# Performance work log

Measured on AMD Instinct MI355X. Metric: run time of the kernel, lower is better.

Reference implementation:

```python
import jax, jax.numpy as jnp
import numpy as np

L, F, LOG_T, NMIN, NMAX = 16, 2, 19, 16, 2048
T = 2 ** LOG_T
N_ROWS = 524288
PRIMES = np.array([1, 2654435761, 805459861], dtype=np.uint32)
# 8 corner offsets of the unit cube, bits (dx, dy, dz)
CORNERS = np.stack(np.meshgrid([0, 1], [0, 1], [0, 1], indexing='ij'), axis=-1).reshape(8, 3)


def setup_inputs() -> dict:
    key = jax.random.key(0)
    k1, k2 = jax.random.split(key)
    x = jax.random.uniform(k1, (N_ROWS, 3), dtype=jnp.float32)  # coords in [0,1)
    hashmap = jax.random.normal(k2, (L, F, T), dtype=jnp.float32) * 1e-2
    growth = np.exp((np.log(NMAX) - np.log(NMIN)) / (L - 1))
    resolution = jnp.asarray(np.floor(NMIN * growth ** np.arange(L)), dtype=jnp.float32)
    return {"x": x, "hashmap": hashmap, "resolution": resolution}


def _hash_encode(x, hashmap, resolution):
    # x: [n, 3], hashmap: [L, F, T], resolution: [L]
    n = x.shape[0]
    xs = x[:, None, :] * resolution[None, :, None]          # [n, L, 3]
    x0f = jnp.floor(xs)
    frac = xs - x0f                                          # trilinear fracs [n, L, 3]
    x0 = x0f.astype(jnp.uint32)

    primes = jnp.asarray(PRIMES)                             # [3] uint32
    h0 = x0 * primes                                         # [n, L, 3] (wraps mod 2^32)
    h1 = (x0 + jnp.uint32(1)) * primes                       # [n, L, 3]
    hpair = jnp.stack([h0, h1], axis=-2)                     # [n, L, 2, 3]

    c = jnp.asarray(CORNERS, dtype=jnp.int32)                # [8, 3]
    # hashed index per corner: xor of per-dim hashes, masked to table size
    idx = (hpair[:, :, c[:, 0], 0]
           ^ hpair[:, :, c[:, 1], 1]
           ^ hpair[:, :, c[:, 2], 2]) & jnp.uint32(T - 1)    # [n, L, 8]

    wpair = jnp.stack([1.0 - frac, frac], axis=-2)           # [n, L, 2, 3]
    w = (wpair[:, :, c[:, 0], 0]
         * wpair[:, :, c[:, 1], 1]
         * wpair[:, :, c[:, 2], 2])                          # [n, L, 8]

    def per_level(hm_l, idx_l, w_l):
        # hm_l: [F, T], idx_l: [n, 8], w_l: [n, 8]
        feats = jnp.take(hm_l, idx_l, axis=1)                # [F, n, 8]
        return jnp.einsum('fnc,nc->nf', feats, w_l)          # [n, F]

    out = jax.vmap(per_level)(hashmap,
                              idx.transpose(1, 0, 2),
                              w.transpose(1, 0, 2))          # [L, n, F]
    # match torch layout: (L,F,n) -> (n, L, F) -> (n, L*F)
    return out.transpose(1, 0, 2).reshape(n, L * F)


def reference(x, hashmap, resolution):
    return _hash_encode(x, hashmap, resolution)
```

## Files before the change

### kernel.cpp

```cpp
#include <hip/hip_runtime.h>
#include <hip/hip_fp16.h>


#define HG_L     16
#define HG_LOG_T 19
#define HG_T     (1u << HG_LOG_T)
#define HG_N     524288u
#define HP1      2654435761u
#define HP2      805459861u

#define DS0 17u
#define DS1 23u
#define DS2 31u
#define DS3 43u
#define DS4 59u
#define DOFF0 0u
#define DOFF1 4913u
#define DOFF2 17080u
#define DOFF3 46871u
#define DOFF4 126378u
#define DTOTAL 331757u
#define TAB_U2 (HG_L * (HG_T / 2u))

__global__ __launch_bounds__(256) void interleave_fp16(
    const float* __restrict__ hm,
    __half2* __restrict__ ws)
{
    const unsigned u = (blockIdx.x * 256u + threadIdx.x) * 4u;
    const unsigned l = u >> HG_LOG_T;
    const unsigned t = u & (HG_T - 1u);
    const float* base = hm + (size_t)l * (2u * HG_T);
    const float4 a = *reinterpret_cast<const float4*>(base + t);
    const float4 b = *reinterpret_cast<const float4*>(base + HG_T + t);
    __half2 h0 = __floats2half2_rn(a.x, b.x);
    __half2 h1 = __floats2half2_rn(a.y, b.y);
    __half2 h2 = __floats2half2_rn(a.z, b.z);
    __half2 h3 = __floats2half2_rn(a.w, b.w);
    uint4 o;
    o.x = *reinterpret_cast<unsigned*>(&h0);
    o.y = *reinterpret_cast<unsigned*>(&h1);
    o.z = *reinterpret_cast<unsigned*>(&h2);
    o.w = *reinterpret_cast<unsigned*>(&h3);
    *reinterpret_cast<uint4*>(ws + u) = o;
}

__global__ __launch_bounds__(256) void build_lattice(
    const float* __restrict__ hm,
    uint2* __restrict__ latD)
{
    const unsigned l = blockIdx.y;
    unsigned S, off;
    switch (l) {
        case 0: S = DS0; off = DOFF0; break;
        case 1: S = DS1; off = DOFF1; break;
        case 2: S = DS2; off = DOFF2; break;
        case 3: S = DS3; off = DOFF3; break;
        default: S = DS4; off = DOFF4; break;
    }
    const unsigned i = blockIdx.x * 256u + threadIdx.x;
    if (i >= S * S * S) return;
    const unsigned x  = i % S;
    const unsigned t1 = i / S;
    const unsigned y  = t1 % S;
    const unsigned z  = t1 / S;
    const unsigned hyz = y * HP1 ^ z * HP2;
    const unsigned i0 = (hyz ^ x) & (HG_T - 1u);
    const unsigned i1 = (hyz ^ (x + 1u)) & (HG_T - 1u);
    const float* b0 = hm + (size_t)l * (2u * HG_T);
    __half2 v0 = __floats2half2_rn(b0[i0], b0[i0 + HG_T]);
    __half2 v1 = __floats2half2_rn(b0[i1], b0[i1 + HG_T]);
    uint2 o;
    o.x = *reinterpret_cast<unsigned*>(&v0);
    o.y = *reinterpret_cast<unsigned*>(&v1);
    latD[off + i] = o;
}

__device__ __forceinline__ float2 hfv(unsigned raw) {
    return __half22float2(*reinterpret_cast<const __half2*>(&raw));
}

template <unsigned S, unsigned OFF>
__device__ __forceinline__ float2 enc_dense(
    float px, float py, float pz, float res,
    const uint2* __restrict__ latD)
{
    const float xs0 = px * res, xs1 = py * res, xs2 = pz * res;
    const float fl0 = floorf(xs0), fl1 = floorf(xs1), fl2 = floorf(xs2);
    const float fr0 = xs0 - fl0, fr1 = xs1 - fl1, fr2 = xs2 - fl2;
    const unsigned x0 = (unsigned)fl0;
    const unsigned y0 = (unsigned)fl1;
    const unsigned z0 = (unsigned)fl2;

    const unsigned i = (z0 * S + y0) * S + x0 + OFF;
    const uint2 q00 = latD[i];
    const uint2 q10 = latD[i + S];
    const uint2 q01 = latD[i + S * S];
    const uint2 q11 = latD[i + S * S + S];

    const float w0x = 1.0f - fr0, w1x = fr0;
    const float w00 = (1.0f - fr1) * (1.0f - fr2);
    const float w10 = fr1 * (1.0f - fr2);
    const float w01 = (1.0f - fr1) * fr2;
    const float w11 = fr1 * fr2;

    const float2 a00 = hfv(q00.x), b00 = hfv(q00.y);
    const float2 a10 = hfv(q10.x), b10 = hfv(q10.y);
    const float2 a01 = hfv(q01.x), b01 = hfv(q01.y);
    const float2 a11 = hfv(q11.x), b11 = hfv(q11.y);

    float ax = 0.0f, ay = 0.0f;
    ax += w00 * (w0x * a00.x + w1x * b00.x);
    ay += w00 * (w0x * a00.y + w1x * b00.y);
    ax += w10 * (w0x * a10.x + w1x * b10.x);
    ay += w10 * (w0x * a10.y + w1x * b10.y);
    ax += w01 * (w0x * a01.x + w1x * b01.x);
    ay += w01 * (w0x * a01.y + w1x * b01.y);
    ax += w11 * (w0x * a11.x + w1x * b11.x);
    ay += w11 * (w0x * a11.y + w1x * b11.y);
    return make_float2(ax, ay);
}

__device__ __forceinline__ float2 enc_hash(
    float px, float py, float pz, float res,
    const uint2* __restrict__ tab2)
{
    const float xs0 = px * res, xs1 = py * res, xs2 = pz * res;
    const float fl0 = floorf(xs0), fl1 = floorf(xs1), fl2 = floorf(xs2);
    const float fr0 = xs0 - fl0, fr1 = xs1 - fl1, fr2 = xs2 - fl2;
    const unsigned x0 = (unsigned)fl0;
    const unsigned y0 = (unsigned)fl1;
    const unsigned z0 = (unsigned)fl2;
    const unsigned M = HG_T - 1u;

    const unsigned hy0 = y0 * HP1, hy1 = hy0 + HP1;
    const unsigned hz0 = z0 * HP2, hz1 = hz0 + HP2;
    const unsigned H0 = hy0 ^ hz0;
    const unsigned H1 = hy1 ^ hz0;
    const unsigned H2 = hy0 ^ hz1;
    const unsigned H3 = hy1 ^ hz1;

    unsigned r0[4], r1[4];
    {
        const unsigned i0 = (H0 ^ x0) & M; const uint2 q = tab2[i0 >> 1];
        r0[0] = (i0 & 1u) ? q.y : q.x;  r1[0] = (i0 & 1u) ? q.x : q.y;
    }
    {
        const unsigned i0 = (H1 ^ x0) & M; const uint2 q = tab2[i0 >> 1];
        r0[1] = (i0 & 1u) ? q.y : q.x;  r1[1] = (i0 & 1u) ? q.x : q.y;
    }
    {
        const unsigned i0 = (H2 ^ x0) & M; const uint2 q = tab2[i0 >> 1];
        r0[2] = (i0 & 1u) ? q.y : q.x;  r1[2] = (i0 & 1u) ? q.x : q.y;
    }
    {
        const unsigned i0 = (H3 ^ x0) & M; const uint2 q = tab2[i0 >> 1];
        r0[3] = (i0 & 1u) ? q.y : q.x;  r1[3] = (i0 & 1u) ? q.x : q.y;
    }
    if (x0 & 1u) {
        const unsigned xp = x0 + 1u;
        {
            const unsigned i1 = (H0 ^ xp) & M; const uint2 q = tab2[i1 >> 1];
            r1[0] = (i1 & 1u) ? q.y : q.x;
        }
        {
            const unsigned i1 = (H1 ^ xp) & M; const uint2 q = tab2[i1 >> 1];
            r1[1] = (i1 & 1u) ? q.y : q.x;
        }
        {
            const unsigned i1 = (H2 ^ xp) & M; const uint2 q = tab2[i1 >> 1];
            r1[2] = (i1 & 1u) ? q.y : q.x;
        }
        {
            const unsigned i1 = (H3 ^ xp) & M; const uint2 q = tab2[i1 >> 1];
            r1[3] = (i1 & 1u) ? q.y : q.x;
        }
    }

    const float w0x = 1.0f - fr0, w1x = fr0;
    const float w00 = (1.0f - fr1) * (1.0f - fr2);
    const float w10 = fr1 * (1.0f - fr2);
    const float w01 = (1.0f - fr1) * fr2;
    const float w11 = fr1 * fr2;

    float ax = 0.0f, ay = 0.0f;
    {
        const float2 v0 = hfv(r0[0]), v1 = hfv(r1[0]);
        ax += w00 * (w0x * v0.x + w1x * v1.x);
        ay += w00 * (w0x * v0.y + w1x * v1.y);
    }
    {
        const float2 v0 = hfv(r0[1]), v1 = hfv(r1[1]);
        ax += w10 * (w0x * v0.x + w1x * v1.x);
        ay += w10 * (w0x * v0.y + w1x * v1.y);
    }
    {
        const float2 v0 = hfv(r0[2]), v1 = hfv(r1[2]);
        ax += w01 * (w0x * v0.x + w1x * v1.x);
        ay += w01 * (w0x * v0.y + w1x * v1.y);
    }
    {
        const float2 v0 = hfv(r0[3]), v1 = hfv(r1[3]);
        ax += w11 * (w0x * v0.x + w1x * v1.x);
        ay += w11 * (w0x * v0.y + w1x * v1.y);
    }
    return make_float2(ax, ay);
}

__global__ __launch_bounds__(256) void hg_main(
    const float* __restrict__ x,
    const uint2* __restrict__ tab2,
    const uint2* __restrict__ latD,
    const float* __restrict__ resolution,
    float*       __restrict__ out)
{
    const unsigned tid = threadIdx.x;
    const unsigned p0  = blockIdx.x * 512u + tid;
    const unsigned p1  = p0 + 256u;

    const float ax0 = x[p0 * 3 + 0], ay0 = x[p0 * 3 + 1], az0 = x[p0 * 3 + 2];
    const float ax1 = x[p1 * 3 + 0], ay1 = x[p1 * 3 + 1], az1 = x[p1 * 3 + 2];

    {
        float2 A0[8], A1[8];
        A0[0] = enc_dense<DS0, DOFF0>(ax0, ay0, az0, resolution[0], latD);
        A1[0] = enc_dense<DS0, DOFF0>(ax1, ay1, az1, resolution[0], latD);
        A0[1] = enc_dense<DS1, DOFF1>(ax0, ay0, az0, resolution[1], latD);
        A1[1] = enc_dense<DS1, DOFF1>(ax1, ay1, az1, resolution[1], latD);
        A0[2] = enc_dense<DS2, DOFF2>(ax0, ay0, az0, resolution[2], latD);
        A1[2] = enc_dense<DS2, DOFF2>(ax1, ay1, az1, resolution[2], latD);
        A0[3] = enc_dense<DS3, DOFF3>(ax0, ay0, az0, resolution[3], latD);
        A1[3] = enc_dense<DS3, DOFF3>(ax1, ay1, az1, resolution[3], latD);
        A0[4] = enc_dense<DS4, DOFF4>(ax0, ay0, az0, resolution[4], latD);
        A1[4] = enc_dense<DS4, DOFF4>(ax1, ay1, az1, resolution[4], latD);
#pragma unroll
        for (int l = 5; l < 8; ++l) {
            const float res = resolution[l];
            const uint2* tl = tab2 + (size_t)l * (HG_T / 2u);
            A0[l] = enc_hash(ax0, ay0, az0, res, tl);
            A1[l] = enc_hash(ax1, ay1, az1, res, tl);
        }
        float4* d0 = reinterpret_cast<float4*>(out + (size_t)p0 * 32u);
        float4* d1 = reinterpret_cast<float4*>(out + (size_t)p1 * 32u);
        d0[0] = make_float4(A0[0].x, A0[0].y, A0[1].x, A0[1].y);
        d0[1] = make_float4(A0[2].x, A0[2].y, A0[3].x, A0[3].y);
        d0[2] = make_float4(A0[4].x, A0[4].y, A0[5].x, A0[5].y);
        d0[3] = make_float4(A0[6].x, A0[6].y, A0[7].x, A0[7].y);
        d1[0] = make_float4(A1[0].x, A1[0].y, A1[1].x, A1[1].y);
        d1[1] = make_float4(A1[2].x, A1[2].y, A1[3].x, A1[3].y);
        d1[2] = make_float4(A1[4].x, A1[4].y, A1[5].x, A1[5].y);
        d1[3] = make_float4(A1[6].x, A1[6].y, A1[7].x, A1[7].y);
    }
    {
        float2 A0[8], A1[8];
#pragma unroll
        for (int l = 8; l < 16; ++l) {
            const float res = resolution[l];
            const uint2* tl = tab2 + (size_t)l * (HG_T / 2u);
            A0[l - 8] = enc_hash(ax0, ay0, az0, res, tl);
            A1[l - 8] = enc_hash(ax1, ay1, az1, res, tl);
        }
        float4* d0 = reinterpret_cast<float4*>(out + (size_t)p0 * 32u + 16u);
        float4* d1 = reinterpret_cast<float4*>(out + (size_t)p1 * 32u + 16u);
        d0[0] = make_float4(A0[0].x, A0[0].y, A0[1].x, A0[1].y);
        d0[1] = make_float4(A0[2].x, A0[2].y, A0[3].x, A0[3].y);
        d0[2] = make_float4(A0[4].x, A0[4].y, A0[5].x, A0[5].y);
        d0[3] = make_float4(A0[6].x, A0[6].y, A0[7].x, A0[7].y);
        d1[0] = make_float4(A1[0].x, A1[0].y, A1[1].x, A1[1].y);
        d1[1] = make_float4(A1[2].x, A1[2].y, A1[3].x, A1[3].y);
        d1[2] = make_float4(A1[4].x, A1[4].y, A1[5].x, A1[5].y);
        d1[3] = make_float4(A1[6].x, A1[6].y, A1[7].x, A1[7].y);
    }
}

extern "C" void kernel_launch(void* const* d_in, const int* in_sizes, int n_in,
                              void* d_out, int out_size, void* d_ws, size_t ws_size,
                              hipStream_t stream) {
    const float* x          = (const float*)d_in[0];
    const float* hashmap    = (const float*)d_in[1];
    const float* resolution = (const float*)d_in[2];
    float* out              = (float*)d_out;

    __half2* wst  = (__half2*)d_ws;
    uint2*   latD = (uint2*)d_ws + TAB_U2;

    hipLaunchKernelGGL(interleave_fp16,
                       dim3((HG_L * HG_T / 4u) / 256u), dim3(256), 0, stream,
                       hashmap, wst);
    hipLaunchKernelGGL(build_lattice,
                       dim3((DS4 * DS4 * DS4 + 255u) / 256u, 5), dim3(256), 0, stream,
                       hashmap, latD);

    hipLaunchKernelGGL(hg_main, dim3(HG_N / 512u), dim3(256), 0, stream,
                       x, (const uint2*)d_ws, latD, resolution, out);
}
```

Baseline: 348.7 us.

## Store dense lattice as 4-corner quads and extend dense path to level 5

```diff
diff --git a/kernel.cpp b/kernel.cpp
--- a/kernel.cpp
+++ b/kernel.cpp
@@ -14,19 +14,22 @@
 #define DS2 31u
 #define DS3 43u
 #define DS4 59u
+#define DS5 81u
 #define DOFF0 0u
 #define DOFF1 4913u
 #define DOFF2 17080u
 #define DOFF3 46871u
 #define DOFF4 126378u
-#define DTOTAL 331757u
-#define TAB_U2 (HG_L * (HG_T / 2u))
+#define DOFF5 331757u
+#define DTOTAL 863198u
+
+#define TAB_BYTES ((size_t)HG_L * HG_T * 4u)
 
 __global__ __launch_bounds__(256) void interleave_fp16(
     const float* __restrict__ hm,
     __half2* __restrict__ ws)
 {
-    const unsigned u = (blockIdx.x * 256u + threadIdx.x) * 4u;
+    const unsigned u = 6u * HG_T + (blockIdx.x * 256u + threadIdx.x) * 4u;
     const unsigned l = u >> HG_LOG_T;
     const unsigned t = u & (HG_T - 1u);
     const float* base = hm + (size_t)l * (2u * HG_T);
@@ -44,9 +47,14 @@
     *reinterpret_cast<uint4*>(ws + u) = o;
 }
 
-__global__ __launch_bounds__(256) void build_lattice(
+__device__ __forceinline__ unsigned pack_h2(float f0, float f1) {
+    __half2 h = __floats2half2_rn(f0, f1);
+    return *reinterpret_cast<unsigned*>(&h);
+}
+
+__global__ __launch_bounds__(256) void build_quad(
     const float* __restrict__ hm,
-    uint2* __restrict__ latD)
+    uint4* __restrict__ quad)
 {
     const unsigned l = blockIdx.y;
     unsigned S, off;
@@ -55,7 +63,8 @@
         case 1: S = DS1; off = DOFF1; break;
         case 2: S = DS2; off = DOFF2; break;
         case 3: S = DS3; off = DOFF3; break;
-        default: S = DS4; off = DOFF4; break;
+        case 4: S = DS4; off = DOFF4; break;
+        default: S = DS5; off = DOFF5; break;
     }
     const unsigned i = blockIdx.x * 256u + threadIdx.x;
     if (i >= S * S * S) return;
@@ -63,16 +72,20 @@
     const unsigned t1 = i / S;
     const unsigned y  = t1 % S;
     const unsigned z  = t1 / S;
-    const unsigned hyz = y * HP1 ^ z * HP2;
-    const unsigned i0 = (hyz ^ x) & (HG_T - 1u);
-    const unsigned i1 = (hyz ^ (x + 1u)) & (HG_T - 1u);
+    const unsigned M = HG_T - 1u;
+    const unsigned hz = z * HP2;
+    const unsigned hy0 = y * HP1, hy1 = hy0 + HP1;
+    const unsigned i00 = (hy0 ^ hz ^ x) & M;
+    const unsigned i10 = (hy0 ^ hz ^ (x + 1u)) & M;
+    const unsigned i01 = (hy1 ^ hz ^ x) & M;
+    const unsigned i11 = (hy1 ^ hz ^ (x + 1u)) & M;
     const float* b0 = hm + (size_t)l * (2u * HG_T);
-    __half2 v0 = __floats2half2_rn(b0[i0], b0[i0 + HG_T]);
-    __half2 v1 = __floats2half2_rn(b0[i1], b0[i1 + HG_T]);
-    uint2 o;
-    o.x = *reinterpret_cast<unsigned*>(&v0);
-    o.y = *reinterpret_cast<unsigned*>(&v1);
-    latD[off + i] = o;
+    uint4 o;
+    o.x = pack_h2(b0[i00], b0[i00 + HG_T]);
+    o.y = pack_h2(b0[i10], b0[i10 + HG_T]);
+    o.z = pack_h2(b0[i01], b0[i01 + HG_T]);
+    o.w = pack_h2(b0[i11], b0[i11 + HG_T]);
+    quad[off + i] = o;
 }
 
 __device__ __forceinline__ float2 hfv(unsigned raw) {
@@ -82,7 +95,7 @@
 template <unsigned S, unsigned OFF>
 __device__ __forceinline__ float2 enc_dense(
     float px, float py, float pz, float res,
-    const uint2* __restrict__ latD)
+    const uint4* __restrict__ quad)
 {
     const float xs0 = px * res, xs1 = py * res, xs2 = pz * res;
     const float fl0 = floorf(xs0), fl1 = floorf(xs1), fl2 = floorf(xs2);
@@ -92,32 +105,22 @@
     const unsigned z0 = (unsigned)fl2;
 
     const unsigned i = (z0 * S + y0) * S + x0 + OFF;
-    const uint2 q00 = latD[i];
-    const uint2 q10 = latD[i + S];
-    const uint2 q01 = latD[i + S * S];
-    const uint2 q11 = latD[i + S * S + S];
+    const uint4 q0 = quad[i];
+    const uint4 q1 = quad[i + S * S];
 
     const float w0x = 1.0f - fr0, w1x = fr0;
-    const float w00 = (1.0f - fr1) * (1.0f - fr2);
-    const float w10 = fr1 * (1.0f - fr2);
-    const float w01 = (1.0f - fr1) * fr2;
-    const float w11 = fr1 * fr2;
-
-    const float2 a00 = hfv(q00.x), b00 = hfv(q00.y);
-    const float2 a10 = hfv(q10.x), b10 = hfv(q10.y);
-    const float2 a01 = hfv(q01.x), b01 = hfv(q01.y);
-    const float2 a11 = hfv(q11.x), b11 = hfv(q11.y);
-
-    float ax = 0.0f, ay = 0.0f;
-    ax += w00 * (w0x * a00.x + w1x * b00.x);
-    ay += w00 * (w0x * a00.y + w1x * b00.y);
-    ax += w10 * (w0x * a10.x + w1x * b10.x);
-    ay += w10 * (w0x * a10.y + w1x * b10.y);
-    ax += w01 * (w0x * a01.x + w1x * b01.x);
-    ay += w01 * (w0x * a01.y + w1x * b01.y);
-    ax += w11 * (w0x * a11.x + w1x * b11.x);
-    ay += w11 * (w0x * a11.y + w1x * b11.y);
-    return make_float2(ax, ay);
+    const float w0y = 1.0f - fr1, w1y = fr1;
+    const float w0z = 1.0f - fr2, w1z = fr2;
+
+    const float2 a00 = hfv(q0.x), a10 = hfv(q0.y), a01 = hfv(q0.z), a11 = hfv(q0.w);
+    const float2 b00 = hfv(q1.x), b10 = hfv(q1.y), b01 = hfv(q1.z), b11 = hfv(q1.w);
+
+    const float s0x = w0y * (w0x * a00.x + w1x * a10.x) + w1y * (w0x * a01.x + w1x * a11.x);
+    const float s0y = w0y * (w0x * a00.y + w1x * a10.y) + w1y * (w0x * a01.y + w1x * a11.y);
+    const float s1x = w0y * (w0x * b00.x + w1x * b10.x) + w1y * (w0x * b01.x + w1x * b11.x);
+    const float s1y = w0y * (w0x * b00.y + w1x * b10.y) + w1y * (w0x * b01.y + w1x * b11.y);
+
+    return make_float2(w0z * s0x + w1z * s1x, w0z * s0y + w1z * s1y);
 }
 
 __device__ __forceinline__ float2 enc_hash(
@@ -158,22 +161,14 @@
     }
     if (x0 & 1u) {
         const unsigned xp = x0 + 1u;
-        {
-            const unsigned i1 = (H0 ^ xp) & M; const uint2 q = tab2[i1 >> 1];
-            r1[0] = (i1 & 1u) ? q.y : q.x;
-        }
-        {
-            const unsigned i1 = (H1 ^ xp) & M; const uint2 q = tab2[i1 >> 1];
-            r1[1] = (i1 & 1u) ? q.y : q.x;
-        }
-        {
-            const unsigned i1 = (H2 ^ xp) & M; const uint2 q = tab2[i1 >> 1];
-            r1[2] = (i1 & 1u) ? q.y : q.x;
-        }
-        {
-            const unsigned i1 = (H3 ^ xp) & M; const uint2 q = tab2[i1 >> 1];
-            r1[3] = (i1 & 1u) ? q.y : q.x;
-        }
+        { const unsigned i1 = (H0 ^ xp) & M; const uint2 q = tab2[i1 >> 1];
+          r1[0] = (i1 & 1u) ? q.y : q.x; }
+        { const unsigned i1 = (H1 ^ xp) & M; const uint2 q = tab2[i1 >> 1];
+          r1[1] = (i1 & 1u) ? q.y : q.x; }
+        { const unsigned i1 = (H2 ^ xp) & M; const uint2 q = tab2[i1 >> 1];
+          r1[2] = (i1 & 1u) ? q.y : q.x; }
+        { const unsigned i1 = (H3 ^ xp) & M; const uint2 q = tab2[i1 >> 1];
+          r1[3] = (i1 & 1u) ? q.y : q.x; }
     }
 
     const float w0x = 1.0f - fr0, w1x = fr0;
@@ -183,33 +178,25 @@
     const float w11 = fr1 * fr2;
 
     float ax = 0.0f, ay = 0.0f;
-    {
-        const float2 v0 = hfv(r0[0]), v1 = hfv(r1[0]);
-        ax += w00 * (w0x * v0.x + w1x * v1.x);
-        ay += w00 * (w0x * v0.y + w1x * v1.y);
-    }
-    {
-        const float2 v0 = hfv(r0[1]), v1 = hfv(r1[1]);
-        ax += w10 * (w0x * v0.x + w1x * v1.x);
-        ay += w10 * (w0x * v0.y + w1x * v1.y);
-    }
-    {
-        const float2 v0 = hfv(r0[2]), v1 = hfv(r1[2]);
-        ax += w01 * (w0x * v0.x + w1x * v1.x);
-        ay += w01 * (w0x * v0.y + w1x * v1.y);
-    }
-    {
-        const float2 v0 = hfv(r0[3]), v1 = hfv(r1[3]);
-        ax += w11 * (w0x * v0.x + w1x * v1.x);
-        ay += w11 * (w0x * v0.y + w1x * v1.y);
-    }
+    { const float2 v0 = hfv(r0[0]), v1 = hfv(r1[0]);
+      ax += w00 * (w0x * v0.x + w1x * v1.x);
+      ay += w00 * (w0x * v0.y + w1x * v1.y); }
+    { const float2 v0 = hfv(r0[1]), v1 = hfv(r1[1]);
+      ax += w10 * (w0x * v0.x + w1x * v1.x);
+      ay += w10 * (w0x * v0.y + w1x * v1.y); }
+    { const float2 v0 = hfv(r0[2]), v1 = hfv(r1[2]);
+      ax += w01 * (w0x * v0.x + w1x * v1.x);
+      ay += w01 * (w0x * v0.y + w1x * v1.y); }
+    { const float2 v0 = hfv(r0[3]), v1 = hfv(r1[3]);
+      ax += w11 * (w0x * v0.x + w1x * v1.x);
+      ay += w11 * (w0x * v0.y + w1x * v1.y); }
     return make_float2(ax, ay);
 }
 
 __global__ __launch_bounds__(256) void hg_main(
     const float* __restrict__ x,
     const uint2* __restrict__ tab2,
-    const uint2* __restrict__ latD,
+    const uint4* __restrict__ quad,
     const float* __restrict__ resolution,
     float*       __restrict__ out)
 {
@@ -222,18 +209,20 @@
 
     {
         float2 A0[8], A1[8];
-        A0[0] = enc_dense<DS0, DOFF0>(ax0, ay0, az0, resolution[0], latD);
-        A1[0] = enc_dense<DS0, DOFF0>(ax1, ay1, az1, resolution[0], latD);
-        A0[1] = enc_dense<DS1, DOFF1>(ax0, ay0, az0, resolution[1], latD);
-        A1[1] = enc_dense<DS1, DOFF1>(ax1, ay1, az1, resolution[1], latD);
-        A0[2] = enc_dense<DS2, DOFF2>(ax0, ay0, az0, resolution[2], latD);
-        A1[2] = enc_dense<DS2, DOFF2>(ax1, ay1, az1, resolution[2], latD);
-        A0[3] = enc_dense<DS3, DOFF3>(ax0, ay0, az0, resolution[3], latD);
-        A1[3] = enc_dense<DS3, DOFF3>(ax1, ay1, az1, resolution[3], latD);
-        A0[4] = enc_dense<DS4, DOFF4>(ax0, ay0, az0, resolution[4], latD);
-        A1[4] = enc_dense<DS4, DOFF4>(ax1, ay1, az1, resolution[4], latD);
+        A0[0] = enc_dense<DS0, DOFF0>(ax0, ay0, az0, resolution[0], quad);
+        A1[0] = enc_dense<DS0, DOFF0>(ax1, ay1, az1, resolution[0], quad);
+        A0[1] = enc_dense<DS1, DOFF1>(ax0, ay0, az0, resolution[1], quad);
+        A1[1] = enc_dense<DS1, DOFF1>(ax1, ay1, az1, resolution[1], quad);
+        A0[2] = enc_dense<DS2, DOFF2>(ax0, ay0, az0, resolution[2], quad);
+        A1[2] = enc_dense<DS2, DOFF2>(ax1, ay1, az1, resolution[2], quad);
+        A0[3] = enc_dense<DS3, DOFF3>(ax0, ay0, az0, resolution[3], quad);
+        A1[3] = enc_dense<DS3, DOFF3>(ax1, ay1, az1, resolution[3], quad);
+        A0[4] = enc_dense<DS4, DOFF4>(ax0, ay0, az0, resolution[4], quad);
+        A1[4] = enc_dense<DS4, DOFF4>(ax1, ay1, az1, resolution[4], quad);
+        A0[5] = enc_dense<DS5, DOFF5>(ax0, ay0, az0, resolution[5], quad);
+        A1[5] = enc_dense<DS5, DOFF5>(ax1, ay1, az1, resolution[5], quad);
 #pragma unroll
-        for (int l = 5; l < 8; ++l) {
+        for (int l = 6; l < 8; ++l) {
             const float res = resolution[l];
             const uint2* tl = tab2 + (size_t)l * (HG_T / 2u);
             A0[l] = enc_hash(ax0, ay0, az0, res, tl);
@@ -281,15 +270,15 @@
     float* out              = (float*)d_out;
 
     __half2* wst  = (__half2*)d_ws;
-    uint2*   latD = (uint2*)d_ws + TAB_U2;
+    uint4*   quad = (uint4*)((char*)d_ws + TAB_BYTES);
 
     hipLaunchKernelGGL(interleave_fp16,
-                       dim3((HG_L * HG_T / 4u) / 256u), dim3(256), 0, stream,
+                       dim3((10u * HG_T / 4u) / 256u), dim3(256), 0, stream,
                        hashmap, wst);
-    hipLaunchKernelGGL(build_lattice,
-                       dim3((DS4 * DS4 * DS4 + 255u) / 256u, 5), dim3(256), 0, stream,
-                       hashmap, latD);
+    hipLaunchKernelGGL(build_quad,
+                       dim3((DS5 * DS5 * DS5 + 255u) / 256u, 6), dim3(256), 0, stream,
+                       hashmap, quad);
 
     hipLaunchKernelGGL(hg_main, dim3(HG_N / 512u), dim3(256), 0, stream,
-                       x, (const uint2*)d_ws, latD, resolution, out);
-}
+                       x, (const uint2*)d_ws, quad, resolution, out);
+}
```

New measurement: 338.0 us. 3.1% less time.
